# Performance work log

Hardware: AMD Instinct MI355X
Metric: run time of the kernel (lower is better)

The kernel has to match this reference:

```python
import jax, jax.numpy as jnp
import numpy as np

N_NODES = 100000
N_EDGES = 1600000
D_FEAT = 48


def setup_inputs() -> dict:
    key = jax.random.key(0)
    k1, k2, k3, k4 = jax.random.split(key, 4)
    rows = jax.random.randint(k1, (N_EDGES,), 0, N_NODES, dtype=jnp.int32)
    cols = jax.random.randint(k2, (N_EDGES,), 0, N_NODES, dtype=jnp.int32)
    vals = jax.random.uniform(k3, (N_EDGES,), dtype=jnp.float32)
    embeds = jax.random.normal(k4, (N_NODES, D_FEAT), dtype=jnp.float32)
    return {"rows": rows, "cols": cols, "vals": vals, "embeds": embeds}


def reference(rows, cols, vals, embeds):
    # out = spmm(adj, embeds): out[r] = sum_{e: rows[e]==r} vals[e] * embeds[cols[e]]
    msgs = vals[:, None] * embeds[cols]  # [E, d] gather + scale
    out = jax.ops.segment_sum(msgs, rows, num_segments=embeds.shape[0])  # [N, d]
    return out
```

## Files before the change

### kernel.cpp

```cpp
#include <hip/hip_runtime.h>
#include <hip/hip_fp16.h>


#define N_NODES 100000
#define N_EDGES 1600000
#define D_FEAT  48

#define R_PER_BUCKET 256
#define NBUCKETS ((N_NODES + R_PER_BUCKET - 1) / R_PER_BUCKET)
#define NWG 512
#define CHUNK ((N_EDGES + NWG - 1) / NWG)
#define MAT (NBUCKETS * NWG)
#define SCAN_CHUNK 1024
#define NB_SCAN ((MAT + SCAN_CHUNK - 1) / SCAN_CHUNK)

__global__ __launch_bounds__(512) void count_kernel(const int* __restrict__ rows,
                                                    unsigned int* __restrict__ mat) {
    __shared__ unsigned int lc[NBUCKETS];
    const int w = blockIdx.x, t = threadIdx.x;
    for (int i = t; i < NBUCKETS; i += 512) lc[i] = 0u;
    __syncthreads();
    const int lo = w * CHUNK;
    const int hi = (lo + CHUNK < N_EDGES) ? lo + CHUNK : N_EDGES;
    for (int e = lo + t; e < hi; e += 512)
        atomicAdd(&lc[rows[e] >> 8], 1u);
    __syncthreads();
    for (int b = t; b < NBUCKETS; b += 512)
        mat[b * NWG + w] = lc[b];
}

__global__ __launch_bounds__(256) void scan_phase1(const unsigned int* __restrict__ mat,
                                                   unsigned int* __restrict__ bsum) {
    __shared__ unsigned int s[256];
    const int blk = blockIdx.x, t = threadIdx.x;
    const int base = blk * SCAN_CHUNK + t * 4;
    unsigned int sum = 0;
#pragma unroll
    for (int k = 0; k < 4; ++k) {
        int i = base + k;
        if (i < MAT) sum += mat[i];
    }
    s[t] = sum;
    __syncthreads();
    for (int off = 128; off > 0; off >>= 1) {
        if (t < off) s[t] += s[t + off];
        __syncthreads();
    }
    if (t == 0) bsum[blk] = s[0];
}

__global__ __launch_bounds__(256) void scan_phase3(unsigned int* __restrict__ mat,
                                                   const unsigned int* __restrict__ bsum,
                                                   unsigned int* __restrict__ bstart) {
    __shared__ unsigned int s[256];
    __shared__ unsigned int bpre[256];
    const int blk = blockIdx.x, t = threadIdx.x;
    bpre[t] = (t < NB_SCAN) ? bsum[t] : 0u;
    __syncthreads();
    for (int off = 1; off < 256; off <<= 1) {
        unsigned int u = (t >= off) ? bpre[t - off] : 0u;
        __syncthreads();
        bpre[t] += u;
        __syncthreads();
    }
    const unsigned int blkbase = (blk == 0) ? 0u : bpre[blk - 1];

    const int base = blk * SCAN_CHUNK + t * 4;
    unsigned int c[4];
    unsigned int sum = 0;
#pragma unroll
    for (int k = 0; k < 4; ++k) {
        int i = base + k;
        c[k] = (i < MAT) ? mat[i] : 0u;
        sum += c[k];
    }
    s[t] = sum;
    __syncthreads();
    for (int off = 1; off < 256; off <<= 1) {
        unsigned int u = (t >= off) ? s[t - off] : 0u;
        __syncthreads();
        s[t] += u;
        __syncthreads();
    }
    unsigned int prefix = blkbase + ((t == 0) ? 0u : s[t - 1]);
#pragma unroll
    for (int k = 0; k < 4; ++k) {
        int i = base + k;
        if (i < MAT) {
            mat[i] = prefix;
            if ((i & (NWG - 1)) == 0) bstart[i / NWG] = prefix;
            prefix += c[k];
        }
    }
    if (blk == 0 && t == 0) bstart[NBUCKETS] = N_EDGES;
}

__global__ __launch_bounds__(512) void place_kernel(const int* __restrict__ rows,
                                                    const int* __restrict__ cols,
                                                    const float* __restrict__ vals,
                                                    const unsigned int* __restrict__ mat,
                                                    int2* __restrict__ buf1) {
    __shared__ unsigned int lc[NBUCKETS];
    const int w = blockIdx.x, t = threadIdx.x;
    for (int b = t; b < NBUCKETS; b += 512) lc[b] = mat[b * NWG + w];
    __syncthreads();
    const int lo = w * CHUNK;
    const int hi = (lo + CHUNK < N_EDGES) ? lo + CHUNK : N_EDGES;
    for (int e = lo + t; e < hi; e += 512) {
        int r = rows[e];
        unsigned int pos = atomicAdd(&lc[r >> 8], 1u);
        buf1[pos] = make_int2(((r & 255) << 17) | cols[e], __float_as_int(vals[e]));
    }
}

__global__ __launch_bounds__(512) void bucket_finalize(const unsigned int* __restrict__ bstart,
                                                       const int2* __restrict__ buf1,
                                                       unsigned int* __restrict__ buf2,
                                                       unsigned int* __restrict__ offsets) {
    __shared__ unsigned int rc[R_PER_BUCKET];
    __shared__ unsigned int s[R_PER_BUCKET];
    const int b = blockIdx.x, t = threadIdx.x;
    const unsigned int S = bstart[b];
    const unsigned int E = bstart[b + 1];
    if (t < R_PER_BUCKET) rc[t] = 0u;
    __syncthreads();
    for (unsigned int j = S + t; j < E; j += 512)
        atomicAdd(&rc[(unsigned)buf1[j].x >> 17], 1u);
    __syncthreads();
    if (t < R_PER_BUCKET) s[t] = rc[t];
    __syncthreads();
    for (int off = 1; off < R_PER_BUCKET; off <<= 1) {
        unsigned int u = 0;
        if (t < R_PER_BUCKET && t >= off) u = s[t - off];
        __syncthreads();
        if (t < R_PER_BUCKET && t >= off) s[t] += u;
        __syncthreads();
    }
    const int row0 = b * R_PER_BUCKET;
    if (t < R_PER_BUCKET) {
        unsigned int pre = (t == 0) ? 0u : s[t - 1];
        int row = row0 + t;
        if (row < N_NODES) offsets[row] = S + pre;
        rc[t] = S + pre;
    }
    if (b == NBUCKETS - 1 && t == 0) offsets[N_NODES] = N_EDGES;
    __syncthreads();
    for (unsigned int j = S + t; j < E; j += 512) {
        int2 cv = buf1[j];
        unsigned int pos = atomicAdd(&rc[(unsigned)cv.x >> 17], 1u);
        union { __half h; unsigned short u; } hv;
        hv.h = __float2half_rn(__int_as_float(cv.y));
        buf2[pos] = ((unsigned int)hv.u << 17) | ((unsigned)cv.x & 0x1FFFFu);
    }
}

__global__ __launch_bounds__(256) void convert_embeds(const float4* __restrict__ src,
                                                      __half2* __restrict__ dst, int n4) {
    int i = blockIdx.x * 256 + threadIdx.x;
    if (i < n4) {
        float4 v = src[i];
        dst[2 * i]     = __floats2half2_rn(v.x, v.y);
        dst[2 * i + 1] = __floats2half2_rn(v.z, v.w);
    }
}

__global__ __launch_bounds__(256) void spmm_kernel(const unsigned int* __restrict__ offsets,
                                                   const unsigned int* __restrict__ colval,
                                                   const __half2* __restrict__ embeds_h2,
                                                   float* __restrict__ out) {
    const int t   = threadIdx.x;
    const int grp = t >> 5;
    const int sub = t & 31;
    const int row = blockIdx.x * 8 + grp;
    if (row >= N_NODES) return;

    unsigned int j   = offsets[row];
    unsigned int end = offsets[row + 1];
    const bool act = sub < 24;
    float ax = 0.f, ay = 0.f;

#define PROC(q)                                                            \
    {                                                                      \
        union { __half h; unsigned short u; } hv;                          \
        hv.u = (unsigned short)((q) >> 17);                                \
        float vv = __half2float(hv.h);                                     \
        __half2 e2 = embeds_h2[((q) & 0x1FFFFu) * 24 + sub];               \
        ax = fmaf(vv, __low2float(e2), ax);                                \
        ay = fmaf(vv, __high2float(e2), ay);                               \
    }

    for (; j + 8 <= end; j += 8) {
        unsigned int q0 = colval[j + 0];
        unsigned int q1 = colval[j + 1];
        unsigned int q2 = colval[j + 2];
        unsigned int q3 = colval[j + 3];
        unsigned int q4 = colval[j + 4];
        unsigned int q5 = colval[j + 5];
        unsigned int q6 = colval[j + 6];
        unsigned int q7 = colval[j + 7];
        if (act) {
            PROC(q0) PROC(q1) PROC(q2) PROC(q3)
            PROC(q4) PROC(q5) PROC(q6) PROC(q7)
        }
    }
    for (; j + 4 <= end; j += 4) {
        unsigned int q0 = colval[j + 0];
        unsigned int q1 = colval[j + 1];
        unsigned int q2 = colval[j + 2];
        unsigned int q3 = colval[j + 3];
        if (act) { PROC(q0) PROC(q1) PROC(q2) PROC(q3) }
    }
    for (; j < end; ++j) {
        unsigned int q = colval[j];
        if (act) PROC(q)
    }
#undef PROC

    if (act) {
        float2 o;
        o.x = ax;
        o.y = ay;
        *(float2*)(out + (size_t)row * D_FEAT + sub * 2) = o;
    }
}

__global__ __launch_bounds__(256) void zero_out_kernel(float4* __restrict__ out, int n4) {
    int i = blockIdx.x * 256 + threadIdx.x;
    if (i < n4) out[i] = make_float4(0.f, 0.f, 0.f, 0.f);
}
__global__ __launch_bounds__(256) void spmm_atomic_kernel(const int* __restrict__ rows,
                                                          const int* __restrict__ cols,
                                                          const float* __restrict__ vals,
                                                          const float* __restrict__ embeds,
                                                          float* __restrict__ out) {
    long long tid = (long long)blockIdx.x * 256 + threadIdx.x;
    const long long total = (long long)N_EDGES * 12;
    if (tid >= total) return;
    int e = (int)(tid / 12), q = (int)(tid % 12);
    int r = rows[e], c = cols[e];
    float v = vals[e];
    const float4 emb = *(const float4*)(embeds + (long long)c * D_FEAT + q * 4);
    float* o = out + (long long)r * D_FEAT + q * 4;
    atomicAdd(o + 0, v * emb.x);
    atomicAdd(o + 1, v * emb.y);
    atomicAdd(o + 2, v * emb.z);
    atomicAdd(o + 3, v * emb.w);
}

extern "C" void kernel_launch(void* const* d_in, const int* in_sizes, int n_in,
                              void* d_out, int out_size, void* d_ws, size_t ws_size,
                              hipStream_t stream) {
    const int*   rows   = (const int*)d_in[0];
    const int*   cols   = (const int*)d_in[1];
    const float* vals   = (const float*)d_in[2];
    const float* embeds = (const float*)d_in[3];
    float*       out    = (float*)d_out;

    unsigned int* mat     = (unsigned int*)d_ws;
    unsigned int* offsets = (unsigned int*)d_ws;
    size_t mat_bytes  = ((size_t)MAT * 4 + 15) & ~(size_t)15;
    unsigned int* bstart = (unsigned int*)((char*)d_ws + mat_bytes);
    size_t bs_bytes   = (((size_t)(NBUCKETS + 1) * 4) + 15) & ~(size_t)15;
    unsigned int* bsum = (unsigned int*)((char*)d_ws + mat_bytes + bs_bytes);
    size_t bsum_bytes = (((size_t)NB_SCAN * 4) + 15) & ~(size_t)15;
    char* buf1_base = (char*)d_ws + mat_bytes + bs_bytes + bsum_bytes;
    int2* buf1 = (int2*)buf1_base;
    __half* embeds_h = (__half*)buf1_base;
    unsigned int* buf2 = (unsigned int*)(buf1_base + (size_t)N_EDGES * 8);
    size_t need = mat_bytes + bs_bytes + bsum_bytes +
                  (size_t)N_EDGES * 8 + (size_t)N_EDGES * 4;

    if (ws_size < need) {
        int n4 = out_size / 4;
        zero_out_kernel<<<(n4 + 255) / 256, 256, 0, stream>>>((float4*)out, n4);
        long long total = (long long)N_EDGES * 12;
        spmm_atomic_kernel<<<(int)((total + 255) / 256), 256, 0, stream>>>(rows, cols, vals, embeds, out);
        return;
    }

    count_kernel<<<NWG, 512, 0, stream>>>(rows, mat);
    scan_phase1<<<NB_SCAN, 256, 0, stream>>>(mat, bsum);
    scan_phase3<<<NB_SCAN, 256, 0, stream>>>(mat, bsum, bstart);
    place_kernel<<<NWG, 512, 0, stream>>>(rows, cols, vals, mat, buf1);
    bucket_finalize<<<NBUCKETS, 512, 0, stream>>>(bstart, buf1, buf2, offsets);
    int n4e = (N_NODES * D_FEAT) / 4;
    convert_embeds<<<(n4e + 255) / 256, 256, 0, stream>>>((const float4*)embeds,
                                                          (__half2*)embeds_h, n4e);
    spmm_kernel<<<(N_NODES + 7) / 8, 256, 0, stream>>>(offsets, buf2,
                                                       (const __half2*)embeds_h, out);
}
```

Before: 94.59 us.

## Fuse bucket finalize with SpMM via shared-memory CSR and merge embed conversion into count

Bucket finalization and SpMM now run in one kernel: each block sorts its bucket's edges by row into shared memory, then computes output rows straight from that local CSR. This removes the global buf2 and offsets round-trip and one launch. The embedding fp16 conversion moves into the count kernel as extra blocks, removing another launch. Bucket size drops to 128 rows and NWG to 256 to fit the shared capacity, with a slow fallback path when a bucket exceeds that capacity.

```diff
diff --git a/kernel.cpp b/kernel.cpp
--- a/kernel.cpp
+++ b/kernel.cpp
@@ -6,27 +6,42 @@
 #define N_EDGES 1600000
 #define D_FEAT  48
 
-#define R_PER_BUCKET 256
+#define R_PER_BUCKET 128
 #define NBUCKETS ((N_NODES + R_PER_BUCKET - 1) / R_PER_BUCKET)
-#define NWG 512
+#define NWG 256
 #define CHUNK ((N_EDGES + NWG - 1) / NWG)
 #define MAT (NBUCKETS * NWG)
 #define SCAN_CHUNK 1024
 #define NB_SCAN ((MAT + SCAN_CHUNK - 1) / SCAN_CHUNK)
-
-__global__ __launch_bounds__(512) void count_kernel(const int* __restrict__ rows,
-                                                    unsigned int* __restrict__ mat) {
-    __shared__ unsigned int lc[NBUCKETS];
-    const int w = blockIdx.x, t = threadIdx.x;
-    for (int i = t; i < NBUCKETS; i += 512) lc[i] = 0u;
-    __syncthreads();
-    const int lo = w * CHUNK;
-    const int hi = (lo + CHUNK < N_EDGES) ? lo + CHUNK : N_EDGES;
-    for (int e = lo + t; e < hi; e += 512)
-        atomicAdd(&lc[rows[e] >> 8], 1u);
-    __syncthreads();
-    for (int b = t; b < NBUCKETS; b += 512)
-        mat[b * NWG + w] = lc[b];
+#define CONV_N4 ((N_NODES * D_FEAT) / 4)
+#define CONV_BLK ((CONV_N4 + 511) / 512)
+#define CAP 3072
+
+__global__ __launch_bounds__(512) void count_convert(const int* __restrict__ rows,
+                                                     unsigned int* __restrict__ mat,
+                                                     const float4* __restrict__ esrc,
+                                                     __half2* __restrict__ edst) {
+    const int t = threadIdx.x;
+    if (blockIdx.x < NWG) {
+        __shared__ unsigned int lc[NBUCKETS];
+        const int w = blockIdx.x;
+        for (int i = t; i < NBUCKETS; i += 512) lc[i] = 0u;
+        __syncthreads();
+        const int lo = w * CHUNK;
+        const int hi = (lo + CHUNK < N_EDGES) ? lo + CHUNK : N_EDGES;
+        for (int e = lo + t; e < hi; e += 512)
+            atomicAdd(&lc[rows[e] >> 7], 1u);
+        __syncthreads();
+        for (int b = t; b < NBUCKETS; b += 512)
+            mat[b * NWG + w] = lc[b];
+    } else {
+        int i = (blockIdx.x - NWG) * 512 + t;
+        if (i < CONV_N4) {
+            float4 v = esrc[i];
+            edst[2 * i]     = __floats2half2_rn(v.x, v.y);
+            edst[2 * i + 1] = __floats2half2_rn(v.z, v.w);
+        }
+    }
 }
 
 __global__ __launch_bounds__(256) void scan_phase1(const unsigned int* __restrict__ mat,
@@ -108,120 +123,114 @@
     const int hi = (lo + CHUNK < N_EDGES) ? lo + CHUNK : N_EDGES;
     for (int e = lo + t; e < hi; e += 512) {
         int r = rows[e];
-        unsigned int pos = atomicAdd(&lc[r >> 8], 1u);
-        buf1[pos] = make_int2(((r & 255) << 17) | cols[e], __float_as_int(vals[e]));
-    }
-}
-
-__global__ __launch_bounds__(512) void bucket_finalize(const unsigned int* __restrict__ bstart,
-                                                       const int2* __restrict__ buf1,
-                                                       unsigned int* __restrict__ buf2,
-                                                       unsigned int* __restrict__ offsets) {
+        unsigned int pos = atomicAdd(&lc[r >> 7], 1u);
+        buf1[pos] = make_int2(((r & 127) << 17) | cols[e], __float_as_int(vals[e]));
+    }
+}
+
+__global__ __launch_bounds__(512) void finalize_spmm(const unsigned int* __restrict__ bstart,
+                                                     const int2* __restrict__ buf1,
+                                                     const __half2* __restrict__ embeds_h2,
+                                                     float* __restrict__ out) {
+    __shared__ unsigned int sedge[CAP];
+    __shared__ unsigned int rstart[R_PER_BUCKET + 1];
     __shared__ unsigned int rc[R_PER_BUCKET];
-    __shared__ unsigned int s[R_PER_BUCKET];
+    __shared__ unsigned int sscan[R_PER_BUCKET];
     const int b = blockIdx.x, t = threadIdx.x;
     const unsigned int S = bstart[b];
     const unsigned int E = bstart[b + 1];
-    if (t < R_PER_BUCKET) rc[t] = 0u;
-    __syncthreads();
-    for (unsigned int j = S + t; j < E; j += 512)
-        atomicAdd(&rc[(unsigned)buf1[j].x >> 17], 1u);
-    __syncthreads();
-    if (t < R_PER_BUCKET) s[t] = rc[t];
-    __syncthreads();
-    for (int off = 1; off < R_PER_BUCKET; off <<= 1) {
-        unsigned int u = 0;
-        if (t < R_PER_BUCKET && t >= off) u = s[t - off];
-        __syncthreads();
-        if (t < R_PER_BUCKET && t >= off) s[t] += u;
-        __syncthreads();
-    }
+    const unsigned int cnt = E - S;
+    const int g   = t >> 5;
+    const int sub = t & 31;
+    const bool act = sub < 24;
     const int row0 = b * R_PER_BUCKET;
-    if (t < R_PER_BUCKET) {
-        unsigned int pre = (t == 0) ? 0u : s[t - 1];
-        int row = row0 + t;
-        if (row < N_NODES) offsets[row] = S + pre;
-        rc[t] = S + pre;
-    }
-    if (b == NBUCKETS - 1 && t == 0) offsets[N_NODES] = N_EDGES;
-    __syncthreads();
-    for (unsigned int j = S + t; j < E; j += 512) {
-        int2 cv = buf1[j];
-        unsigned int pos = atomicAdd(&rc[(unsigned)cv.x >> 17], 1u);
-        union { __half h; unsigned short u; } hv;
-        hv.h = __float2half_rn(__int_as_float(cv.y));
-        buf2[pos] = ((unsigned int)hv.u << 17) | ((unsigned)cv.x & 0x1FFFFu);
-    }
-}
-
-__global__ __launch_bounds__(256) void convert_embeds(const float4* __restrict__ src,
-                                                      __half2* __restrict__ dst, int n4) {
-    int i = blockIdx.x * 256 + threadIdx.x;
-    if (i < n4) {
-        float4 v = src[i];
-        dst[2 * i]     = __floats2half2_rn(v.x, v.y);
-        dst[2 * i + 1] = __floats2half2_rn(v.z, v.w);
-    }
-}
-
-__global__ __launch_bounds__(256) void spmm_kernel(const unsigned int* __restrict__ offsets,
-                                                   const unsigned int* __restrict__ colval,
-                                                   const __half2* __restrict__ embeds_h2,
-                                                   float* __restrict__ out) {
-    const int t   = threadIdx.x;
-    const int grp = t >> 5;
-    const int sub = t & 31;
-    const int row = blockIdx.x * 8 + grp;
-    if (row >= N_NODES) return;
-
-    unsigned int j   = offsets[row];
-    unsigned int end = offsets[row + 1];
-    const bool act = sub < 24;
-    float ax = 0.f, ay = 0.f;
-
-#define PROC(q)                                                            \
-    {                                                                      \
-        union { __half h; unsigned short u; } hv;                          \
-        hv.u = (unsigned short)((q) >> 17);                                \
-        float vv = __half2float(hv.h);                                     \
-        __half2 e2 = embeds_h2[((q) & 0x1FFFFu) * 24 + sub];               \
-        ax = fmaf(vv, __low2float(e2), ax);                                \
-        ay = fmaf(vv, __high2float(e2), ay);                               \
-    }
-
-    for (; j + 8 <= end; j += 8) {
-        unsigned int q0 = colval[j + 0];
-        unsigned int q1 = colval[j + 1];
-        unsigned int q2 = colval[j + 2];
-        unsigned int q3 = colval[j + 3];
-        unsigned int q4 = colval[j + 4];
-        unsigned int q5 = colval[j + 5];
-        unsigned int q6 = colval[j + 6];
-        unsigned int q7 = colval[j + 7];
-        if (act) {
-            PROC(q0) PROC(q1) PROC(q2) PROC(q3)
-            PROC(q4) PROC(q5) PROC(q6) PROC(q7)
-        }
-    }
-    for (; j + 4 <= end; j += 4) {
-        unsigned int q0 = colval[j + 0];
-        unsigned int q1 = colval[j + 1];
-        unsigned int q2 = colval[j + 2];
-        unsigned int q3 = colval[j + 3];
-        if (act) { PROC(q0) PROC(q1) PROC(q2) PROC(q3) }
-    }
-    for (; j < end; ++j) {
-        unsigned int q = colval[j];
-        if (act) PROC(q)
+
+#define PROC(q)                                                       \
+    {                                                                 \
+        union { __half h; unsigned short u; } hv;                     \
+        hv.u = (unsigned short)((q) >> 17);                           \
+        float vv = __half2float(hv.h);                                \
+        __half2 e2 = embeds_h2[((q) & 0x1FFFFu) * 24 + sub];          \
+        ax = fmaf(vv, __low2float(e2), ax);                           \
+        ay = fmaf(vv, __high2float(e2), ay);                          \
+    }
+
+    if (cnt <= CAP) {
+        if (t < R_PER_BUCKET) rc[t] = 0u;
+        __syncthreads();
+        for (unsigned int j = S + t; j < E; j += 512)
+            atomicAdd(&rc[(unsigned)buf1[j].x >> 17], 1u);
+        __syncthreads();
+        if (t < R_PER_BUCKET) sscan[t] = rc[t];
+        __syncthreads();
+        for (int off = 1; off < R_PER_BUCKET; off <<= 1) {
+            unsigned int u = 0;
+            if (t < R_PER_BUCKET && t >= off) u = sscan[t - off];
+            __syncthreads();
+            if (t < R_PER_BUCKET && t >= off) sscan[t] += u;
+            __syncthreads();
+        }
+        if (t < R_PER_BUCKET) {
+            unsigned int pre = (t == 0) ? 0u : sscan[t - 1];
+            rstart[t] = pre;
+            rc[t] = pre;
+        }
+        if (t == 0) rstart[R_PER_BUCKET] = cnt;
+        __syncthreads();
+        for (unsigned int j = S + t; j < E; j += 512) {
+            int2 cv = buf1[j];
+            unsigned int pos = atomicAdd(&rc[(unsigned)cv.x >> 17], 1u);
+            union { __half h; unsigned short u; } hv;
+            hv.h = __float2half_rn(__int_as_float(cv.y));
+            sedge[pos] = ((unsigned int)hv.u << 17) | ((unsigned)cv.x & 0x1FFFFu);
+        }
+        __syncthreads();
+
+        for (int rr = g * 8; rr < g * 8 + 8; ++rr) {
+            int row = row0 + rr;
+            if (row >= N_NODES) break;
+            unsigned int j = rstart[rr], end = rstart[rr + 1];
+            float ax = 0.f, ay = 0.f;
+            for (; j + 8 <= end; j += 8) {
+                unsigned int q0 = sedge[j + 0];
+                unsigned int q1 = sedge[j + 1];
+                unsigned int q2 = sedge[j + 2];
+                unsigned int q3 = sedge[j + 3];
+                unsigned int q4 = sedge[j + 4];
+                unsigned int q5 = sedge[j + 5];
+                unsigned int q6 = sedge[j + 6];
+                unsigned int q7 = sedge[j + 7];
+                if (act) {
+                    PROC(q0) PROC(q1) PROC(q2) PROC(q3)
+                    PROC(q4) PROC(q5) PROC(q6) PROC(q7)
+                }
+            }
+            for (; j < end; ++j) {
+                unsigned int q = sedge[j];
+                if (act) PROC(q)
+            }
+            if (act)
+                *(float2*)(out + (size_t)row * D_FEAT + sub * 2) = make_float2(ax, ay);
+        }
+    } else {
+        for (int rr = g * 8; rr < g * 8 + 8; ++rr) {
+            int row = row0 + rr;
+            if (row >= N_NODES) break;
+            float ax = 0.f, ay = 0.f;
+            for (unsigned int j = S; j < E; ++j) {
+                int2 cv = buf1[j];
+                if (((unsigned)cv.x >> 17) == (unsigned)rr && act) {
+                    union { __half h; unsigned short u; } hv;
+                    hv.h = __float2half_rn(__int_as_float(cv.y));
+                    unsigned int q = ((unsigned int)hv.u << 17) | ((unsigned)cv.x & 0x1FFFFu);
+                    PROC(q)
+                }
+            }
+            if (act)
+                *(float2*)(out + (size_t)row * D_FEAT + sub * 2) = make_float2(ax, ay);
+        }
     }
 #undef PROC
-
-    if (act) {
-        float2 o;
-        o.x = ax;
-        o.y = ay;
-        *(float2*)(out + (size_t)row * D_FEAT + sub * 2) = o;
-    }
 }
 
 __global__ __launch_bounds__(256) void zero_out_kernel(float4* __restrict__ out, int n4) {
@@ -256,19 +265,16 @@
     const float* embeds = (const float*)d_in[3];
     float*       out    = (float*)d_out;
 
-    unsigned int* mat     = (unsigned int*)d_ws;
-    unsigned int* offsets = (unsigned int*)d_ws;
+    unsigned int* mat = (unsigned int*)d_ws;
     size_t mat_bytes  = ((size_t)MAT * 4 + 15) & ~(size_t)15;
     unsigned int* bstart = (unsigned int*)((char*)d_ws + mat_bytes);
     size_t bs_bytes   = (((size_t)(NBUCKETS + 1) * 4) + 15) & ~(size_t)15;
     unsigned int* bsum = (unsigned int*)((char*)d_ws + mat_bytes + bs_bytes);
     size_t bsum_bytes = (((size_t)NB_SCAN * 4) + 15) & ~(size_t)15;
-    char* buf1_base = (char*)d_ws + mat_bytes + bs_bytes + bsum_bytes;
-    int2* buf1 = (int2*)buf1_base;
-    __half* embeds_h = (__half*)buf1_base;
-    unsigned int* buf2 = (unsigned int*)(buf1_base + (size_t)N_EDGES * 8);
+    int2* buf1 = (int2*)((char*)d_ws + mat_bytes + bs_bytes + bsum_bytes);
+    __half2* embeds_h2 = (__half2*)((char*)buf1 + (size_t)N_EDGES * 8);
     size_t need = mat_bytes + bs_bytes + bsum_bytes +
-                  (size_t)N_EDGES * 8 + (size_t)N_EDGES * 4;
+                  (size_t)N_EDGES * 8 + (size_t)N_NODES * D_FEAT * 2;
 
     if (ws_size < need) {
         int n4 = out_size / 4;
@@ -278,14 +284,10 @@
         return;
     }
 
-    count_kernel<<<NWG, 512, 0, stream>>>(rows, mat);
+    count_convert<<<NWG + CONV_BLK, 512, 0, stream>>>(rows, mat,
+                                                      (const float4*)embeds, embeds_h2);
     scan_phase1<<<NB_SCAN, 256, 0, stream>>>(mat, bsum);
     scan_phase3<<<NB_SCAN, 256, 0, stream>>>(mat, bsum, bstart);
     place_kernel<<<NWG, 512, 0, stream>>>(rows, cols, vals, mat, buf1);
-    bucket_finalize<<<NBUCKETS, 512, 0, stream>>>(bstart, buf1, buf2, offsets);
-    int n4e = (N_NODES * D_FEAT) / 4;
-    convert_embeds<<<(n4e + 255) / 256, 256, 0, stream>>>((const float4*)embeds,
-                                                          (__half2*)embeds_h, n4e);
-    spmm_kernel<<<(N_NODES + 7) / 8, 256, 0, stream>>>(offsets, buf2,
-                                                       (const __half2*)embeds_h, out);
-}
+    finalize_spmm<<<NBUCKETS, 512, 0, stream>>>(bstart, buf1, embeds_h2, out);
+}
```

New measurement: 81.50 us. 13.8% less time.
